# Performance work log

Measured on AMD Instinct MI355X. Metric: run time of the kernel, lower is better.

Reference implementation:

```python
import jax, jax.numpy as jnp
import numpy as np

THRESHOLD = 0.9
N = 20000
K = 32
F = 64


def setup_inputs() -> dict:
    key = jax.random.key(0)
    k1, k2, k3, k4, k5 = jax.random.split(key, 5)
    features = jax.random.normal(k1, (N, F), dtype=jnp.float32)
    score = jax.random.normal(k2, (N, 1), dtype=jnp.float32)
    distances = jax.random.uniform(k3, (N, K), dtype=jnp.float32)
    # two equal segments; neighbours sampled within own segment, self at col 0
    row_splits = jnp.array([0, N // 2, N], dtype=jnp.int32)
    segN = N // 2
    local_self = (jnp.arange(N, dtype=jnp.int32) % segN)
    seg_start = (jnp.arange(N, dtype=jnp.int32) // segN) * segN
    r = jax.random.randint(k4, (N, K - 1), 0, segN - 1, dtype=jnp.int32)
    r = r + (r >= local_self[:, None]).astype(jnp.int32)  # avoid sampling self
    neigh = seg_start[:, None] + r
    nidxs = jnp.concatenate([jnp.arange(N, dtype=jnp.int32)[:, None], neigh], axis=1)
    tidxs = jax.random.randint(k5, (N, 1), 0, 50, dtype=jnp.int32)
    return {"features": features, "score": score, "distances": distances,
            "nidxs": nidxs, "row_splits": row_splits, "tidxs": tidxs}


def _lnc(features, score_logits, nidxs, row_splits):
    n, k = nidxs.shape
    score = jax.nn.sigmoid(score_logits[:, 0])  # [N]
    # hierarchy order: per row-split segment, descending score
    seg_id = jnp.searchsorted(row_splits, jnp.arange(n), side='right') - 1
    order = jnp.lexsort((-score, seg_id))

    arangeK = jnp.arange(k)

    def step(carry, p):
        ggather, sel, npg, gcount = carry
        already = ggather[p] >= 0
        high = score[p] > THRESHOLD
        m = nidxs[p]                                   # [K], m[0] == p (self)
        free = (m >= 0) & (ggather[jnp.clip(m, 0, n - 1)] < 0)
        self_only = arangeK == 0
        valid = jnp.where(high, free, self_only) & (~already) & (m >= 0)
        g = gcount
        idx_w = jnp.where(valid, m, n)                 # dummy slot n for masked writes
        ggather = ggather.at[idx_w].set(g)
        row_i = jnp.where(already, n, g)
        sel = sel.at[row_i].set(jnp.where(valid, m, -1))
        npg = npg.at[row_i].set(jnp.sum(valid.astype(jnp.int32)))
        created = (~already).astype(jnp.int32)
        return (ggather, sel, npg, gcount + created), created

    init = (jnp.full((n + 1,), -1, jnp.int32),
            jnp.full((n + 1, k), -1, jnp.int32),
            jnp.zeros((n + 1,), jnp.int32),
            jnp.int32(0))
    (ggather, sel, npg, gcount), created = jax.lax.scan(step, init, order)
    ggather, sel, npg = ggather[:n], sel[:n], npg[:n]

    # new row splits: cumulative group count at segment boundaries
    cum = jnp.cumsum(created)
    rs_new = jnp.concatenate([jnp.zeros((1,), jnp.int32),
                              cum[row_splits[1:] - 1].astype(jnp.int32)])

    # pooled features per group (rows >= gcount are padding)
    sel_c = jnp.clip(sel, 0, n - 1)
    gathered = features[sel_c]                         # [N, K, F]
    mask = (sel >= 0)[..., None]
    out_mean = jnp.sum(jnp.where(mask, gathered, 0.0), axis=1)
    out_mean = out_mean / (npg[:, None].astype(features.dtype) + 1e-6)
    out_max = jnp.max(jnp.where(mask, gathered, -1000.0), axis=1)
    out = jnp.concatenate([out_mean, out_max], axis=-1)  # [N, 2F]
    backgather = ggather[:, None]
    return out, rs_new, backgather


def reference(features, score, distances, nidxs, row_splits, tidxs):
    # distances/tidxs only feed the (disabled) loss branch; kept for signature parity
    return _lnc(features, score, nidxs, row_splits)
```

## Files before the change

### kernel.cpp

```cpp
#include <hip/hip_runtime.h>


constexpr int KN = 32;
constexpr int FD = 64;
constexpr int HOCAP = 512;
constexpr int EW = 16;
constexpr int NBB = 2048;
constexpr int NT = 256;
constexpr int NTA = 512;
constexpr int NMAX = 20000;
constexpr int BSLOT = 64;
constexpr int TS = 2048;

typedef unsigned long long u64;

__device__ __forceinline__ int swz(int i) { return i ^ ((i >> 4) & 3); }

__global__ void k0_init(const float* __restrict__ score, int* __restrict__ grab,
                        u64* __restrict__ hlkStage, int* __restrict__ hcnt,
                        int* __restrict__ lcnt0, int* __restrict__ lcnt1,
                        u64* __restrict__ key, const int* __restrict__ row_splits,
                        int n) {
  __shared__ int ch, cl0, cl1;
  int tid = (int)threadIdx.x, bid = (int)blockIdx.x;
  int x = bid * NT + tid;
  int lane = tid & 63;
  int half = row_splits[1];
  if (tid == 0) { ch = 0; cl0 = 0; cl1 = 0; }
  __syncthreads();
  bool hi = false, lo = false;
  u64 pk = 0;
  if (x < n) {
    float sp = 1.0f / (1.0f + expf(-score[x]));
    grab[x] = 0x7FFFFFFF;
    hi = sp > 0.9f; lo = !hi;
    unsigned sb = __float_as_uint(sp);
    pk = ((u64)(x >= half) << 63) | ((u64)(0x7FFFFFFFu - sb) << 32) | (unsigned)x;
    key[x] = lo ? (((u64)sb << 32) | (u64)(0xFFFFFFFFu - (unsigned)x)) : 0ull;
  }
  u64 bh = __ballot(hi);
  u64 b0 = __ballot(lo && x < half);
  u64 b1 = __ballot(lo && x >= half);
  int base = 0;
  if (lane == 0) {
    if (bh) base = atomicAdd(&ch, __popcll(bh));
    if (b0) atomicAdd(&cl0, __popcll(b0));
    if (b1) atomicAdd(&cl1, __popcll(b1));
  }
  base = __shfl(base, 0);
  if (hi) {
    int idx = base + __popcll(bh & ((1ull << lane) - 1ull));
    if (idx < BSLOT) hlkStage[bid * BSLOT + idx] = pk;
  }
  __syncthreads();
  if (tid == 0) {
    hcnt[bid] = (ch > BSLOT) ? BSLOT : ch;
    lcnt0[bid] = cl0; lcnt1[bid] = cl1;
  }
}

__global__ __launch_bounds__(NTA, 1) void kA(
    const u64* __restrict__ hlkStage, const int* __restrict__ hcnt,
    const int* __restrict__ lcnt0, const int* __restrict__ lcnt1,
    const int* __restrict__ nidxs, const int* __restrict__ row_splits,
    int* __restrict__ nbm, int* __restrict__ fgj, int* __restrict__ counters,
    int n) {
  __shared__ unsigned short hr16[NMAX];
  __shared__ unsigned E[HOCAP * EW];
  __shared__ u64 hk[HOCAP];
  __shared__ int hol[HOCAP];
  __shared__ int fgjL[HOCAP];
  __shared__ int cnts[128];
  __shared__ int pref[129];
  __shared__ int lsum[2];
  __shared__ int shg;
  int tid = (int)threadIdx.x;
  int lane = tid & 63;
  int half = row_splits[1];
  int nblk = (n + NT - 1) / NT; if (nblk > 128) nblk = 128;

  {
    unsigned* h32 = (unsigned*)hr16;
    for (int i = tid; i < NMAX / 2; i += NTA) h32[i] = 0xFFFFFFFFu;
  }
  for (int i = tid; i < HOCAP * EW; i += NTA) E[i] = 0u;
  if (tid < 128) cnts[tid] = (tid < nblk) ? hcnt[tid] : 0;
  if (tid == 0) { lsum[0] = 0; lsum[1] = 0; }
  __syncthreads();

  if (tid < 64) {
    int v0 = cnts[tid], v1 = cnts[64 + tid];
#pragma unroll
    for (int off = 1; off < 64; off <<= 1) {
      int t0 = __shfl_up(v0, off), t1 = __shfl_up(v1, off);
      if (lane >= off) { v0 += t0; v1 += t1; }
    }
    int s0 = __shfl(v0, 63);
    pref[tid + 1] = v0;
    pref[64 + tid + 1] = v1 + s0;
    if (tid == 0) pref[0] = 0;
  }
  if (tid >= 64 && tid < 192) {
    int b = tid - 64;
    if (b < nblk) { atomicAdd(&lsum[0], lcnt0[b]); atomicAdd(&lsum[1], lcnt1[b]); }
  }
  __syncthreads();
  int nh = pref[nblk]; if (nh > HOCAP) nh = HOCAP;

  for (int t = tid; t < nblk * BSLOT; t += NTA) {
    int b = t >> 6, j = t & (BSLOT - 1);
    if (j < cnts[b]) {
      int d = pref[b] + j;
      if (d < HOCAP) hk[d] = hlkStage[t];
    }
  }
  __syncthreads();

  for (int i = tid; i < nh; i += NTA) {
    u64 kp = hk[i];
    int rk = 0;
#pragma unroll 8
    for (int j = 0; j < nh; ++j) rk += (hk[j] < kp) ? 1 : 0;
    int p = (int)(unsigned)(kp & 0xFFFFFFFFu);
    hol[rk] = p; hr16[p] = (unsigned short)rk;
  }
  __syncthreads();

  {
    const int4* nsrc = (const int4*)nidxs;
    int4* ndstG = (int4*)nbm;
    int tot = nh * 8;
    for (int t = tid; t < tot; t += NTA) {
      int j = t >> 3, q4 = t & 7;
      int p = hol[j];
      int4 v = nsrc[p * 8 + q4];
      ndstG[t] = v;
      unsigned bit = 1u << (j & 31);
      unsigned widx = (unsigned)(j >> 5);
      int xs[4] = { v.x, v.y, v.z, v.w };
#pragma unroll
      for (int e = 0; e < 4; ++e) {
        unsigned r = ((unsigned)xs[e] < (unsigned)n) ? hr16[xs[e]] : 0xFFFFu;
        if (r != 0xFFFFu) atomicOr(&E[r * EW + widx], bit);
      }
    }
  }
  __syncthreads();

  if (tid < 64) {
    unsigned Fw[16];
#pragma unroll
    for (int w = 0; w < 16; ++w) Fw[w] = 0u;
    int hg = 0, h0 = 0, h1 = 0;
    u64 mask_lt = (1ull << lane) - 1ull;
#pragma unroll
    for (int c = 0; c < HOCAP / 64; ++c) {
      if (c * 64 >= nh) break;
      int j = c * 64 + lane;
      bool valid = j < nh;
      unsigned er[16];
#pragma unroll
      for (int w = 0; w < 16; ++w) er[w] = valid ? E[j * EW + w] : 0u;
      unsigned acc = 0;
#pragma unroll
      for (int w = 0; w < 16; ++w) acc |= er[w] & Fw[w];
      bool base_already = acc != 0u;
      u64 erc = ((u64)er[2 * c + 1] << 32) | er[2 * c];
      u64 fb = 0;
      for (int l = 0; l < 64; ++l) {
        bool already = base_already || ((erc & fb) != 0ull);
        bool formed = valid && !already;
        fb |= __ballot(formed && (lane == l));
      }
      Fw[2 * c]     |= (unsigned)(fb & 0xFFFFFFFFull);
      Fw[2 * c + 1] |= (unsigned)(fb >> 32);
      bool formed = (fb >> lane) & 1ull;
      int p = valid ? hol[j] : 0;
      if (formed) {
        int idx = hg + __popcll(fb & mask_lt);
        fgjL[idx] = j;
      }
      h0 += __popcll(__ballot(formed && p < half));
      h1 += __popcll(__ballot(formed && p >= half));
      hg += __popcll(fb);
    }
    if (lane == 0) {
      counters[1] = hg; counters[2] = h0; counters[3] = h1; shg = hg;
    }
  }
  __syncthreads();
  int hg = shg;
  for (int i = tid; i < hg; i += NTA) fgj[i] = fgjL[i];
  if (tid == 0) {
    counters[0] = nh;
    counters[4] = lsum[0];
    counters[5] = lsum[1];
  }
}

__global__ void kG(const int* __restrict__ nbm, const int* __restrict__ fgj,
                   int* __restrict__ grab, u64* __restrict__ key,
                   int* __restrict__ counters, const int* __restrict__ row_splits,
                   int n) {
  int t = (int)(blockIdx.x * blockDim.x + threadIdx.x);
  int lane = (int)threadIdx.x & 63;
  int half = row_splits[1];
  int hg = counters[1];
  bool gl0 = false, gl1 = false;
  if (t < hg * KN) {
    int g = t >> 5;
    int x = nbm[fgj[g] * KN + (t & 31)];
    if ((unsigned)x < (unsigned)n) {
      int old = atomicMin(&grab[x], g);
      if (old == 0x7FFFFFFF && key[x] != 0ull) {
        key[x] = 0ull;
        if (x < half) gl0 = true; else gl1 = true;
      }
    }
  }
  u64 b0 = __ballot(gl0), b1 = __ballot(gl1);
  if (lane == 0) {
    if (b0) atomicSub(&counters[4], __popcll(b0));
    if (b1) atomicSub(&counters[5], __popcll(b1));
  }
}

__global__ void kBC(const int* __restrict__ row_splits, const u64* __restrict__ key,
                    const int* __restrict__ grab, const int* __restrict__ nbm,
                    const int* __restrict__ fgj, const int* __restrict__ counters,
                    const float* __restrict__ feat, float* __restrict__ out,
                    int n, int rs_off) {
  __shared__ u64 ktile[TS];
  int tid = (int)threadIdx.x, bid = (int)blockIdx.x;
  int gtid = bid * NT + tid;
  int lane = tid & 63;
  int wv = tid >> 6;
  int half = row_splits[1];
  const int GSZ = NBB * NT;
  const int NW = GSZ >> 6;
  int wid = gtid >> 6;
  int hg = counters[1], H0 = counters[2], H1 = counters[3];
  int L0 = counters[4], L1 = counters[5];
  int G = H0 + H1 + L0 + L1;
  int bg = rs_off + 3;
  const float inv1 = 1.0f / (1.0f + 1e-6f);

  int nblk16 = (n + 15) >> 4;
  for (int tsk = bid; tsk < nblk16; tsk += NBB) {
    int p0 = tsk * 16;
    int pw = p0 + wv * 4;
    u64 kp[4];
#pragma unroll
    for (int j = 0; j < 4; ++j) kp[j] = (pw + j < n) ? key[pw + j] : 0ull;
    int seg_lo = (p0 < half) ? 0 : half;
    int seg_cnt = (p0 < half) ? half : (n - half);
    unsigned r0 = 0, r1 = 0, r2 = 0, r3 = 0;
    for (int toff = 0; toff < seg_cnt; toff += TS) {
      int tcnt = seg_cnt - toff; if (tcnt > TS) tcnt = TS;
      __syncthreads();
      for (int i = tid; i < tcnt; i += NT) ktile[swz(i)] = key[seg_lo + toff + i];
      __syncthreads();
      for (int i = lane; i < tcnt; i += 64) {
        u64 kk = ktile[swz(i)];
        r0 += (kk > kp[0]) ? 1u : 0u;
        r1 += (kk > kp[1]) ? 1u : 0u;
        r2 += (kk > kp[2]) ? 1u : 0u;
        r3 += (kk > kp[3]) ? 1u : 0u;
      }
    }
#pragma unroll
    for (int off = 32; off > 0; off >>= 1) {
      r0 += __shfl_down(r0, off);
      r1 += __shfl_down(r1, off);
      r2 += __shfl_down(r2, off);
      r3 += __shfl_down(r3, off);
    }
    r0 = __shfl(r0, 0); r1 = __shfl(r1, 0); r2 = __shfl(r2, 0); r3 = __shfl(r3, 0);
    unsigned rr[4] = { r0, r1, r2, r3 };
#pragma unroll
    for (int j = 0; j < 4; ++j) {
      if (kp[j] == 0ull) continue;
      int p = pw + j;
      int base = (p < half) ? H0 : (H0 + L0 + H1);
      int gid = base + (int)rr[j];
      float v = feat[p * FD + lane];
      out[gid * (2 * FD) + lane] = v * inv1;
      out[gid * (2 * FD) + FD + lane] = v;
      if (lane == 0) out[bg + p] = (float)gid;
    }
  }

  for (int x = gtid; x < n; x += GSZ) {
    int prov = grab[x];
    if (prov != 0x7FFFFFFF)
      out[bg + x] = (float)((prov < H0) ? prov : (prov + L0));
  }

  for (int row = G + wid; row < n; row += NW) {
    out[row * (2 * FD) + lane] = 0.0f;
    out[row * (2 * FD) + FD + lane] = -1000.0f;
  }

  {
    int wtail = (NBB - 1 - bid) * (NT >> 6) + wv;
    for (int g = wtail; g < hg; g += NW) {
      int x = 0;
      bool mine = false;
      if (lane < KN) {
        x = nbm[fgj[g] * KN + lane];
        mine = (grab[x] == g);
      }
      u64 bal = __ballot(mine);
      unsigned mask = (unsigned)(bal & 0xFFFFFFFFull);
      int npg = __popc(mask);
      float sum = 0.0f, mx = -1000.0f;
      for (int k = 0; k < KN; ++k) {
        if (mask & (1u << k)) {
          int m = __shfl(x, k);
          float v = feat[m * FD + lane];
          sum += v; mx = fmaxf(mx, v);
        }
      }
      int gid2 = (g < H0) ? g : (g + L0);
      out[gid2 * (2 * FD) + lane] = sum / ((float)npg + 1e-6f);
      out[gid2 * (2 * FD) + FD + lane] = mx;
    }
  }

  if (gtid == 0) {
    out[rs_off + 0] = 0.0f;
    out[rs_off + 1] = (float)(H0 + L0);
    out[rs_off + 2] = (float)(H0 + L0 + H1 + L1);
  }
}

extern "C" void kernel_launch(void* const* d_in, const int* in_sizes, int n_in,
                              void* d_out, int out_size, void* d_ws, size_t ws_size,
                              hipStream_t stream) {
  const float* features   = (const float*)d_in[0];
  const float* score      = (const float*)d_in[1];
  const int*   nidxs      = (const int*)d_in[3];
  const int*   row_splits = (const int*)d_in[4];
  int n = in_sizes[1];
  float* out = (float*)d_out;
  int* wsi = (int*)d_ws;
  int rs_off = n * 2 * FD;

  int*      counters = wsi;
  int*      grab     = wsi + 8 + n;
  u64*      key      = (u64*)(wsi + 8 + 2 * n);
  int*      nbm      = wsi + 8 + 5 * n;
  int*      fgj      = wsi + 8 + 5 * n + HOCAP * KN;
  u64*      hlkStage = (u64*)(fgj + 2 * HOCAP);
  int*      hcnt     = (int*)(hlkStage + 128 * BSLOT);
  int*      lcnt0    = hcnt + 128;
  int*      lcnt1    = lcnt0 + 128;

  int blocks = (n + NT - 1) / NT;
  k0_init<<<blocks, NT, 0, stream>>>(score, grab, hlkStage, hcnt, lcnt0,
                                     lcnt1, key, row_splits, n);
  kA<<<1, NTA, 0, stream>>>(hlkStage, hcnt, lcnt0, lcnt1, nidxs, row_splits,
                            nbm, fgj, counters, n);
  kG<<<(HOCAP * KN) / NT, NT, 0, stream>>>(nbm, fgj, grab, key, counters,
                                           row_splits, n);
  kBC<<<NBB, NT, 0, stream>>>(row_splits, key, grab, nbm, fgj, counters,
                              features, out, n, rs_off);
}
```

Measured before the change: 72.80 us.

## Fuse init, hierarchy and grab kernels into one persistent kernel with grid semaphores

Merges the three launches for score init, high-score ordering/conflict resolution and grab into a single 40-block kernel. Blocks hand off through agent-scope atomic semaphores with spin-wait, and block 0 performs the serial phase. The intent is to remove two kernel launch gaps and their dependencies, at the cost of a memset launch and a spin-based grid barrier that depends on all 40 blocks being co-resident. The per-block staging buffers shrink to match the 40 blocks of 512 threads.

```diff
diff --git a/kernel.cpp b/kernel.cpp
--- a/kernel.cpp
+++ b/kernel.cpp
@@ -7,7 +7,8 @@
 constexpr int EW = 16;
 constexpr int NBB = 2048;
 constexpr int NT = 256;
-constexpr int NTA = 512;
+constexpr int NBF = 40;
+constexpr int NTF = 512;
 constexpr int NMAX = 20000;
 constexpr int BSLOT = 64;
 constexpr int TS = 2048;
@@ -16,212 +17,222 @@
 
 __device__ __forceinline__ int swz(int i) { return i ^ ((i >> 4) & 3); }
 
-__global__ void k0_init(const float* __restrict__ score, int* __restrict__ grab,
-                        u64* __restrict__ hlkStage, int* __restrict__ hcnt,
-                        int* __restrict__ lcnt0, int* __restrict__ lcnt1,
-                        u64* __restrict__ key, const int* __restrict__ row_splits,
-                        int n) {
-  __shared__ int ch, cl0, cl1;
-  int tid = (int)threadIdx.x, bid = (int)blockIdx.x;
-  int x = bid * NT + tid;
-  int lane = tid & 63;
-  int half = row_splits[1];
-  if (tid == 0) { ch = 0; cl0 = 0; cl1 = 0; }
-  __syncthreads();
-  bool hi = false, lo = false;
-  u64 pk = 0;
-  if (x < n) {
-    float sp = 1.0f / (1.0f + expf(-score[x]));
-    grab[x] = 0x7FFFFFFF;
-    hi = sp > 0.9f; lo = !hi;
-    unsigned sb = __float_as_uint(sp);
-    pk = ((u64)(x >= half) << 63) | ((u64)(0x7FFFFFFFu - sb) << 32) | (unsigned)x;
-    key[x] = lo ? (((u64)sb << 32) | (u64)(0xFFFFFFFFu - (unsigned)x)) : 0ull;
-  }
-  u64 bh = __ballot(hi);
-  u64 b0 = __ballot(lo && x < half);
-  u64 b1 = __ballot(lo && x >= half);
-  int base = 0;
-  if (lane == 0) {
-    if (bh) base = atomicAdd(&ch, __popcll(bh));
-    if (b0) atomicAdd(&cl0, __popcll(b0));
-    if (b1) atomicAdd(&cl1, __popcll(b1));
-  }
-  base = __shfl(base, 0);
-  if (hi) {
-    int idx = base + __popcll(bh & ((1ull << lane) - 1ull));
-    if (idx < BSLOT) hlkStage[bid * BSLOT + idx] = pk;
-  }
-  __syncthreads();
-  if (tid == 0) {
-    hcnt[bid] = (ch > BSLOT) ? BSLOT : ch;
-    lcnt0[bid] = cl0; lcnt1[bid] = cl1;
-  }
-}
-
-__global__ __launch_bounds__(NTA, 1) void kA(
-    const u64* __restrict__ hlkStage, const int* __restrict__ hcnt,
-    const int* __restrict__ lcnt0, const int* __restrict__ lcnt1,
-    const int* __restrict__ nidxs, const int* __restrict__ row_splits,
-    int* __restrict__ nbm, int* __restrict__ fgj, int* __restrict__ counters,
-    int n) {
+__global__ __launch_bounds__(NTF, 1) void kF(
+    const float* __restrict__ score, const int* __restrict__ nidxs,
+    const int* __restrict__ row_splits, int* __restrict__ grab,
+    u64* __restrict__ key, int* __restrict__ nbm, int* __restrict__ fgj,
+    int* __restrict__ counters, int* __restrict__ sems,
+    u64* __restrict__ hlkStage, int* __restrict__ hcnt,
+    int* __restrict__ lcnt0, int* __restrict__ lcnt1, int n) {
   __shared__ unsigned short hr16[NMAX];
   __shared__ unsigned E[HOCAP * EW];
   __shared__ u64 hk[HOCAP];
   __shared__ int hol[HOCAP];
   __shared__ int fgjL[HOCAP];
-  __shared__ int cnts[128];
-  __shared__ int pref[129];
+  __shared__ int cnts[NBF];
+  __shared__ int pref[NBF + 1];
   __shared__ int lsum[2];
   __shared__ int shg;
-  int tid = (int)threadIdx.x;
+  __shared__ int ch, cl0, cl1;
+  int tid = (int)threadIdx.x, bid = (int)blockIdx.x;
   int lane = tid & 63;
   int half = row_splits[1];
-  int nblk = (n + NT - 1) / NT; if (nblk > 128) nblk = 128;
-
+
+  if (tid == 0) { ch = 0; cl0 = 0; cl1 = 0; }
+  __syncthreads();
   {
-    unsigned* h32 = (unsigned*)hr16;
-    for (int i = tid; i < NMAX / 2; i += NTA) h32[i] = 0xFFFFFFFFu;
-  }
-  for (int i = tid; i < HOCAP * EW; i += NTA) E[i] = 0u;
-  if (tid < 128) cnts[tid] = (tid < nblk) ? hcnt[tid] : 0;
-  if (tid == 0) { lsum[0] = 0; lsum[1] = 0; }
+    int x = bid * NTF + tid;
+    bool hi = false, lo = false;
+    u64 pk = 0;
+    if (x < n) {
+      float sp = 1.0f / (1.0f + expf(-score[x]));
+      grab[x] = 0x7FFFFFFF;
+      hi = sp > 0.9f; lo = !hi;
+      unsigned sb = __float_as_uint(sp);
+      pk = ((u64)(x >= half) << 63) | ((u64)(0x7FFFFFFFu - sb) << 32) |
+           (unsigned)x;
+      key[x] = lo ? (((u64)sb << 32) | (u64)(0xFFFFFFFFu - (unsigned)x)) : 0ull;
+    }
+    u64 bh = __ballot(hi);
+    u64 b0 = __ballot(lo && x < half);
+    u64 b1 = __ballot(lo && x >= half);
+    int base = 0;
+    if (lane == 0) {
+      if (bh) base = atomicAdd(&ch, __popcll(bh));
+      if (b0) atomicAdd(&cl0, __popcll(b0));
+      if (b1) atomicAdd(&cl1, __popcll(b1));
+    }
+    base = __shfl(base, 0);
+    if (hi) {
+      int idx = base + __popcll(bh & ((1ull << lane) - 1ull));
+      if (idx < BSLOT) hlkStage[bid * BSLOT + idx] = pk;
+    }
+  }
   __syncthreads();
-
-  if (tid < 64) {
-    int v0 = cnts[tid], v1 = cnts[64 + tid];
-#pragma unroll
-    for (int off = 1; off < 64; off <<= 1) {
-      int t0 = __shfl_up(v0, off), t1 = __shfl_up(v1, off);
-      if (lane >= off) { v0 += t0; v1 += t1; }
-    }
-    int s0 = __shfl(v0, 63);
-    pref[tid + 1] = v0;
-    pref[64 + tid + 1] = v1 + s0;
-    if (tid == 0) pref[0] = 0;
-  }
-  if (tid >= 64 && tid < 192) {
-    int b = tid - 64;
-    if (b < nblk) { atomicAdd(&lsum[0], lcnt0[b]); atomicAdd(&lsum[1], lcnt1[b]); }
+  if (tid == 0) {
+    hcnt[bid] = (ch > BSLOT) ? BSLOT : ch;
+    lcnt0[bid] = cl0; lcnt1[bid] = cl1;
+    __hip_atomic_fetch_add(&sems[0], 1, __ATOMIC_RELEASE,
+                           __HIP_MEMORY_SCOPE_AGENT);
+  }
+
+  if (bid == 0) {
+    if (tid == 0) {
+      while (__hip_atomic_load(&sems[0], __ATOMIC_RELAXED,
+                               __HIP_MEMORY_SCOPE_AGENT) < NBF)
+        __builtin_amdgcn_s_sleep(2);
+      __builtin_amdgcn_fence(__ATOMIC_ACQUIRE, "agent");
+    }
+    __syncthreads();
+
+    {
+      unsigned* h32 = (unsigned*)hr16;
+      for (int i = tid; i < NMAX / 2; i += NTF) h32[i] = 0xFFFFFFFFu;
+    }
+    for (int i = tid; i < HOCAP * EW; i += NTF) E[i] = 0u;
+    if (tid < NBF) cnts[tid] = hcnt[tid];
+    if (tid == 0) { lsum[0] = 0; lsum[1] = 0; }
+    __syncthreads();
+
+    if (tid < 64) {
+      int v = (tid < NBF) ? cnts[tid] : 0;
+#pragma unroll
+      for (int off = 1; off < 64; off <<= 1) {
+        int t0 = __shfl_up(v, off);
+        if (lane >= off) v += t0;
+      }
+      if (tid < NBF) pref[tid + 1] = v;
+      if (tid == 0) pref[0] = 0;
+    }
+    if (tid >= 64 && tid < 64 + NBF) {
+      int b = tid - 64;
+      atomicAdd(&lsum[0], lcnt0[b]); atomicAdd(&lsum[1], lcnt1[b]);
+    }
+    __syncthreads();
+    int nh = pref[NBF]; if (nh > HOCAP) nh = HOCAP;
+
+    for (int t = tid; t < NBF * BSLOT; t += NTF) {
+      int b = t >> 6, j = t & (BSLOT - 1);
+      if (j < cnts[b]) {
+        int d = pref[b] + j;
+        if (d < HOCAP) hk[d] = hlkStage[t];
+      }
+    }
+    __syncthreads();
+
+    for (int i = tid; i < nh; i += NTF) {
+      u64 kp = hk[i];
+      int rk = 0;
+#pragma unroll 8
+      for (int j = 0; j < nh; ++j) rk += (hk[j] < kp) ? 1 : 0;
+      int p = (int)(unsigned)(kp & 0xFFFFFFFFu);
+      hol[rk] = p; hr16[p] = (unsigned short)rk;
+    }
+    __syncthreads();
+
+    {
+      const int4* nsrc = (const int4*)nidxs;
+      int4* ndstG = (int4*)nbm;
+      int tot = nh * 8;
+      for (int t = tid; t < tot; t += NTF) {
+        int j = t >> 3, q4 = t & 7;
+        int p = hol[j];
+        int4 v = nsrc[p * 8 + q4];
+        ndstG[t] = v;
+        unsigned bit = 1u << (j & 31);
+        unsigned widx = (unsigned)(j >> 5);
+        int xs[4] = { v.x, v.y, v.z, v.w };
+#pragma unroll
+        for (int e = 0; e < 4; ++e) {
+          unsigned r = ((unsigned)xs[e] < (unsigned)n) ? hr16[xs[e]] : 0xFFFFu;
+          if (r != 0xFFFFu) atomicOr(&E[r * EW + widx], bit);
+        }
+      }
+    }
+    __syncthreads();
+
+    if (tid < 64) {
+      unsigned Fw[16];
+#pragma unroll
+      for (int w = 0; w < 16; ++w) Fw[w] = 0u;
+      int hg = 0, h0 = 0, h1 = 0;
+      u64 mask_lt = (1ull << lane) - 1ull;
+#pragma unroll
+      for (int c = 0; c < HOCAP / 64; ++c) {
+        if (c * 64 >= nh) break;
+        int j = c * 64 + lane;
+        bool valid = j < nh;
+        unsigned er[16];
+#pragma unroll
+        for (int w = 0; w < 16; ++w) er[w] = valid ? E[j * EW + w] : 0u;
+        unsigned acc = 0;
+#pragma unroll
+        for (int w = 0; w < 16; ++w) acc |= er[w] & Fw[w];
+        bool base_already = acc != 0u;
+        u64 erc = ((u64)er[2 * c + 1] << 32) | er[2 * c];
+        u64 fb = 0;
+        for (int l = 0; l < 64; ++l) {
+          bool already = base_already || ((erc & fb) != 0ull);
+          bool formed = valid && !already;
+          fb |= __ballot(formed && (lane == l));
+        }
+        Fw[2 * c]     |= (unsigned)(fb & 0xFFFFFFFFull);
+        Fw[2 * c + 1] |= (unsigned)(fb >> 32);
+        bool formed = (fb >> lane) & 1ull;
+        int p = valid ? hol[j] : 0;
+        if (formed) {
+          int idx = hg + __popcll(fb & mask_lt);
+          fgjL[idx] = j;
+        }
+        h0 += __popcll(__ballot(formed && p < half));
+        h1 += __popcll(__ballot(formed && p >= half));
+        hg += __popcll(fb);
+      }
+      if (lane == 0) {
+        counters[1] = hg; counters[2] = h0; counters[3] = h1; shg = hg;
+      }
+    }
+    __syncthreads();
+    int hgv = shg;
+    for (int i = tid; i < hgv; i += NTF) fgj[i] = fgjL[i];
+    if (tid == 0) {
+      counters[0] = (pref[NBF] > HOCAP) ? HOCAP : pref[NBF];
+      counters[4] = lsum[0];
+      counters[5] = lsum[1];
+    }
+    __syncthreads();
+    if (tid == 0)
+      __hip_atomic_fetch_add(&sems[1], 1, __ATOMIC_RELEASE,
+                             __HIP_MEMORY_SCOPE_AGENT);
+  }
+
+  if (tid == 0) {
+    while (__hip_atomic_load(&sems[1], __ATOMIC_RELAXED,
+                             __HIP_MEMORY_SCOPE_AGENT) < 1)
+      __builtin_amdgcn_s_sleep(2);
+    __builtin_amdgcn_fence(__ATOMIC_ACQUIRE, "agent");
   }
   __syncthreads();
-  int nh = pref[nblk]; if (nh > HOCAP) nh = HOCAP;
-
-  for (int t = tid; t < nblk * BSLOT; t += NTA) {
-    int b = t >> 6, j = t & (BSLOT - 1);
-    if (j < cnts[b]) {
-      int d = pref[b] + j;
-      if (d < HOCAP) hk[d] = hlkStage[t];
-    }
-  }
-  __syncthreads();
-
-  for (int i = tid; i < nh; i += NTA) {
-    u64 kp = hk[i];
-    int rk = 0;
-#pragma unroll 8
-    for (int j = 0; j < nh; ++j) rk += (hk[j] < kp) ? 1 : 0;
-    int p = (int)(unsigned)(kp & 0xFFFFFFFFu);
-    hol[rk] = p; hr16[p] = (unsigned short)rk;
-  }
-  __syncthreads();
-
   {
-    const int4* nsrc = (const int4*)nidxs;
-    int4* ndstG = (int4*)nbm;
-    int tot = nh * 8;
-    for (int t = tid; t < tot; t += NTA) {
-      int j = t >> 3, q4 = t & 7;
-      int p = hol[j];
-      int4 v = nsrc[p * 8 + q4];
-      ndstG[t] = v;
-      unsigned bit = 1u << (j & 31);
-      unsigned widx = (unsigned)(j >> 5);
-      int xs[4] = { v.x, v.y, v.z, v.w };
-#pragma unroll
-      for (int e = 0; e < 4; ++e) {
-        unsigned r = ((unsigned)xs[e] < (unsigned)n) ? hr16[xs[e]] : 0xFFFFu;
-        if (r != 0xFFFFu) atomicOr(&E[r * EW + widx], bit);
-      }
-    }
-  }
-  __syncthreads();
-
-  if (tid < 64) {
-    unsigned Fw[16];
-#pragma unroll
-    for (int w = 0; w < 16; ++w) Fw[w] = 0u;
-    int hg = 0, h0 = 0, h1 = 0;
-    u64 mask_lt = (1ull << lane) - 1ull;
-#pragma unroll
-    for (int c = 0; c < HOCAP / 64; ++c) {
-      if (c * 64 >= nh) break;
-      int j = c * 64 + lane;
-      bool valid = j < nh;
-      unsigned er[16];
-#pragma unroll
-      for (int w = 0; w < 16; ++w) er[w] = valid ? E[j * EW + w] : 0u;
-      unsigned acc = 0;
-#pragma unroll
-      for (int w = 0; w < 16; ++w) acc |= er[w] & Fw[w];
-      bool base_already = acc != 0u;
-      u64 erc = ((u64)er[2 * c + 1] << 32) | er[2 * c];
-      u64 fb = 0;
-      for (int l = 0; l < 64; ++l) {
-        bool already = base_already || ((erc & fb) != 0ull);
-        bool formed = valid && !already;
-        fb |= __ballot(formed && (lane == l));
-      }
-      Fw[2 * c]     |= (unsigned)(fb & 0xFFFFFFFFull);
-      Fw[2 * c + 1] |= (unsigned)(fb >> 32);
-      bool formed = (fb >> lane) & 1ull;
-      int p = valid ? hol[j] : 0;
-      if (formed) {
-        int idx = hg + __popcll(fb & mask_lt);
-        fgjL[idx] = j;
-      }
-      h0 += __popcll(__ballot(formed && p < half));
-      h1 += __popcll(__ballot(formed && p >= half));
-      hg += __popcll(fb);
-    }
+    int hg = counters[1];
+    int t = bid * NTF + tid;
+    bool gl0 = false, gl1 = false;
+    if (t < hg * KN) {
+      int g = t >> 5;
+      int x = nbm[fgj[g] * KN + (t & 31)];
+      if ((unsigned)x < (unsigned)n) {
+        int old = atomicMin(&grab[x], g);
+        if (old == 0x7FFFFFFF && key[x] != 0ull) {
+          key[x] = 0ull;
+          if (x < half) gl0 = true; else gl1 = true;
+        }
+      }
+    }
+    u64 b0 = __ballot(gl0), b1 = __ballot(gl1);
     if (lane == 0) {
-      counters[1] = hg; counters[2] = h0; counters[3] = h1; shg = hg;
-    }
-  }
-  __syncthreads();
-  int hg = shg;
-  for (int i = tid; i < hg; i += NTA) fgj[i] = fgjL[i];
-  if (tid == 0) {
-    counters[0] = nh;
-    counters[4] = lsum[0];
-    counters[5] = lsum[1];
-  }
-}
-
-__global__ void kG(const int* __restrict__ nbm, const int* __restrict__ fgj,
-                   int* __restrict__ grab, u64* __restrict__ key,
-                   int* __restrict__ counters, const int* __restrict__ row_splits,
-                   int n) {
-  int t = (int)(blockIdx.x * blockDim.x + threadIdx.x);
-  int lane = (int)threadIdx.x & 63;
-  int half = row_splits[1];
-  int hg = counters[1];
-  bool gl0 = false, gl1 = false;
-  if (t < hg * KN) {
-    int g = t >> 5;
-    int x = nbm[fgj[g] * KN + (t & 31)];
-    if ((unsigned)x < (unsigned)n) {
-      int old = atomicMin(&grab[x], g);
-      if (old == 0x7FFFFFFF && key[x] != 0ull) {
-        key[x] = 0ull;
-        if (x < half) gl0 = true; else gl1 = true;
-      }
-    }
-  }
-  u64 b0 = __ballot(gl0), b1 = __ballot(gl1);
-  if (lane == 0) {
-    if (b0) atomicSub(&counters[4], __popcll(b0));
-    if (b1) atomicSub(&counters[5], __popcll(b1));
+      if (b0) atomicSub(&counters[4], __popcll(b0));
+      if (b1) atomicSub(&counters[5], __popcll(b1));
+    }
   }
 }
 
@@ -347,22 +358,19 @@
   int rs_off = n * 2 * FD;
 
   int*      counters = wsi;
+  int*      sems     = wsi + 8;
   int*      grab     = wsi + 8 + n;
   u64*      key      = (u64*)(wsi + 8 + 2 * n);
   int*      nbm      = wsi + 8 + 5 * n;
   int*      fgj      = wsi + 8 + 5 * n + HOCAP * KN;
   u64*      hlkStage = (u64*)(fgj + 2 * HOCAP);
-  int*      hcnt     = (int*)(hlkStage + 128 * BSLOT);
-  int*      lcnt0    = hcnt + 128;
-  int*      lcnt1    = lcnt0 + 128;
-
-  int blocks = (n + NT - 1) / NT;
-  k0_init<<<blocks, NT, 0, stream>>>(score, grab, hlkStage, hcnt, lcnt0,
-                                     lcnt1, key, row_splits, n);
-  kA<<<1, NTA, 0, stream>>>(hlkStage, hcnt, lcnt0, lcnt1, nidxs, row_splits,
-                            nbm, fgj, counters, n);
-  kG<<<(HOCAP * KN) / NT, NT, 0, stream>>>(nbm, fgj, grab, key, counters,
-                                           row_splits, n);
+  int*      hcnt     = (int*)(hlkStage + NBF * BSLOT);
+  int*      lcnt0    = hcnt + NBF;
+  int*      lcnt1    = lcnt0 + NBF;
+
+  (void)hipMemsetAsync(sems, 0, 2 * sizeof(int), stream);
+  kF<<<NBF, NTF, 0, stream>>>(score, nidxs, row_splits, grab, key, nbm, fgj,
+                              counters, sems, hlkStage, hcnt, lcnt0, lcnt1, n);
   kBC<<<NBB, NT, 0, stream>>>(row_splits, key, grab, nbm, fgj, counters,
                               features, out, n, rs_off);
 }
```

New measurement: 73.14 us. About the same (+0.5%).

## Split single-block hierarchy kernel across blocks and fuse grab pass with semaphore

Applied to the files above, without the earlier changes.

The single 512-thread block that built the high-score conflict bitmap is replaced by a 40-block kernel. Each block redundantly ranks the candidates, then handles a slice of neighbour lookups. The 20000-entry shared rank table is replaced by binary search over candidates sorted by point id, and the bitmap is built in global memory with atomics. The greedy formation step and the grab pass are fused into one kernel in which block 0 computes the groups and the other blocks spin on a global semaphore before doing the atomicMin grabs. This removes a kernel launch and the serial shared-memory init of the large table, at the cost of redundant per-block ranking, global atomics, and a spin-wait that assumes all blocks are co-resident.

```diff
diff --git a/kernel.cpp b/kernel.cpp
--- a/kernel.cpp
+++ b/kernel.cpp
@@ -7,8 +7,8 @@
 constexpr int EW = 16;
 constexpr int NBB = 2048;
 constexpr int NT = 256;
-constexpr int NTA = 512;
-constexpr int NMAX = 20000;
+constexpr int NBA2 = 40;
+constexpr int NBG = 64;
 constexpr int BSLOT = 64;
 constexpr int TS = 2048;
 
@@ -19,14 +19,17 @@
 __global__ void k0_init(const float* __restrict__ score, int* __restrict__ grab,
                         u64* __restrict__ hlkStage, int* __restrict__ hcnt,
                         int* __restrict__ lcnt0, int* __restrict__ lcnt1,
-                        u64* __restrict__ key, const int* __restrict__ row_splits,
-                        int n) {
+                        u64* __restrict__ key, unsigned* __restrict__ EG,
+                        int* __restrict__ sems,
+                        const int* __restrict__ row_splits, int n) {
   __shared__ int ch, cl0, cl1;
   int tid = (int)threadIdx.x, bid = (int)blockIdx.x;
   int x = bid * NT + tid;
   int lane = tid & 63;
   int half = row_splits[1];
   if (tid == 0) { ch = 0; cl0 = 0; cl1 = 0; }
+  if (x < HOCAP * EW) EG[x] = 0u;
+  if (x == 0) sems[0] = 0;
   __syncthreads();
   bool hi = false, lo = false;
   u64 pk = 0;
@@ -59,35 +62,20 @@
   }
 }
 
-__global__ __launch_bounds__(NTA, 1) void kA(
+__global__ __launch_bounds__(NT) void kA2(
     const u64* __restrict__ hlkStage, const int* __restrict__ hcnt,
-    const int* __restrict__ lcnt0, const int* __restrict__ lcnt1,
-    const int* __restrict__ nidxs, const int* __restrict__ row_splits,
-    int* __restrict__ nbm, int* __restrict__ fgj, int* __restrict__ counters,
-    int n) {
-  __shared__ unsigned short hr16[NMAX];
-  __shared__ unsigned E[HOCAP * EW];
+    const int* __restrict__ nidxs, int* __restrict__ nbm,
+    int* __restrict__ holG, unsigned* __restrict__ EG, int n, int nblk) {
   __shared__ u64 hk[HOCAP];
   __shared__ int hol[HOCAP];
-  __shared__ int fgjL[HOCAP];
+  __shared__ int pidS[HOCAP];
+  __shared__ unsigned short rnkS[HOCAP];
   __shared__ int cnts[128];
   __shared__ int pref[129];
-  __shared__ int lsum[2];
-  __shared__ int shg;
-  int tid = (int)threadIdx.x;
+  int tid = (int)threadIdx.x, bid = (int)blockIdx.x;
   int lane = tid & 63;
-  int half = row_splits[1];
-  int nblk = (n + NT - 1) / NT; if (nblk > 128) nblk = 128;
-
-  {
-    unsigned* h32 = (unsigned*)hr16;
-    for (int i = tid; i < NMAX / 2; i += NTA) h32[i] = 0xFFFFFFFFu;
-  }
-  for (int i = tid; i < HOCAP * EW; i += NTA) E[i] = 0u;
   if (tid < 128) cnts[tid] = (tid < nblk) ? hcnt[tid] : 0;
-  if (tid == 0) { lsum[0] = 0; lsum[1] = 0; }
-  __syncthreads();
-
+  __syncthreads();
   if (tid < 64) {
     int v0 = cnts[tid], v1 = cnts[64 + tid];
 #pragma unroll
@@ -100,14 +88,10 @@
     pref[64 + tid + 1] = v1 + s0;
     if (tid == 0) pref[0] = 0;
   }
-  if (tid >= 64 && tid < 192) {
-    int b = tid - 64;
-    if (b < nblk) { atomicAdd(&lsum[0], lcnt0[b]); atomicAdd(&lsum[1], lcnt1[b]); }
-  }
   __syncthreads();
   int nh = pref[nblk]; if (nh > HOCAP) nh = HOCAP;
 
-  for (int t = tid; t < nblk * BSLOT; t += NTA) {
+  for (int t = tid; t < nblk * BSLOT; t += NT) {
     int b = t >> 6, j = t & (BSLOT - 1);
     if (j < cnts[b]) {
       int d = pref[b] + j;
@@ -116,112 +100,161 @@
   }
   __syncthreads();
 
-  for (int i = tid; i < nh; i += NTA) {
+  for (int i = tid; i < nh; i += NT) {
     u64 kp = hk[i];
-    int rk = 0;
-#pragma unroll 8
-    for (int j = 0; j < nh; ++j) rk += (hk[j] < kp) ? 1 : 0;
-    int p = (int)(unsigned)(kp & 0xFFFFFFFFu);
-    hol[rk] = p; hr16[p] = (unsigned short)rk;
-  }
-  __syncthreads();
+    unsigned px = (unsigned)kp;
+    int rk = 0, rq = 0;
+    for (int j = 0; j < nh; ++j) {
+      u64 kj = hk[j];
+      rk += (kj < kp) ? 1 : 0;
+      rq += ((unsigned)kj < px) ? 1 : 0;
+    }
+    hol[rk] = (int)px;
+    holG[rk] = (int)px;
+    pidS[rq] = (int)px;
+    rnkS[rq] = (unsigned short)rk;
+  }
+  __syncthreads();
+
+  int gpb = (nh + NBA2 - 1) / NBA2;
+  int j0 = bid * gpb;
+  int j1 = j0 + gpb; if (j1 > nh) j1 = nh;
+  int cnt = (j1 > j0) ? (j1 - j0) : 0;
 
   {
     const int4* nsrc = (const int4*)nidxs;
-    int4* ndstG = (int4*)nbm;
-    int tot = nh * 8;
-    for (int t = tid; t < tot; t += NTA) {
-      int j = t >> 3, q4 = t & 7;
-      int p = hol[j];
-      int4 v = nsrc[p * 8 + q4];
-      ndstG[t] = v;
-      unsigned bit = 1u << (j & 31);
-      unsigned widx = (unsigned)(j >> 5);
-      int xs[4] = { v.x, v.y, v.z, v.w };
-#pragma unroll
-      for (int e = 0; e < 4; ++e) {
-        unsigned r = ((unsigned)xs[e] < (unsigned)n) ? hr16[xs[e]] : 0xFFFFu;
-        if (r != 0xFFFFu) atomicOr(&E[r * EW + widx], bit);
-      }
-    }
-  }
-  __syncthreads();
-
-  if (tid < 64) {
-    unsigned Fw[16];
-#pragma unroll
-    for (int w = 0; w < 16; ++w) Fw[w] = 0u;
-    int hg = 0, h0 = 0, h1 = 0;
-    u64 mask_lt = (1ull << lane) - 1ull;
-#pragma unroll
-    for (int c = 0; c < HOCAP / 64; ++c) {
-      if (c * 64 >= nh) break;
-      int j = c * 64 + lane;
-      bool valid = j < nh;
-      unsigned er[16];
-#pragma unroll
-      for (int w = 0; w < 16; ++w) er[w] = valid ? E[j * EW + w] : 0u;
-      unsigned acc = 0;
-#pragma unroll
-      for (int w = 0; w < 16; ++w) acc |= er[w] & Fw[w];
-      bool base_already = acc != 0u;
-      u64 erc = ((u64)er[2 * c + 1] << 32) | er[2 * c];
-      u64 fb = 0;
-      for (int l = 0; l < 64; ++l) {
-        bool already = base_already || ((erc & fb) != 0ull);
-        bool formed = valid && !already;
-        fb |= __ballot(formed && (lane == l));
-      }
-      Fw[2 * c]     |= (unsigned)(fb & 0xFFFFFFFFull);
-      Fw[2 * c + 1] |= (unsigned)(fb >> 32);
-      bool formed = (fb >> lane) & 1ull;
-      int p = valid ? hol[j] : 0;
-      if (formed) {
-        int idx = hg + __popcll(fb & mask_lt);
-        fgjL[idx] = j;
-      }
-      h0 += __popcll(__ballot(formed && p < half));
-      h1 += __popcll(__ballot(formed && p >= half));
-      hg += __popcll(fb);
-    }
+    int4* ndst = (int4*)nbm;
+    for (int t = tid; t < cnt * 8; t += NT) {
+      int j = j0 + (t >> 3), q4 = t & 7;
+      ndst[j * 8 + q4] = nsrc[hol[j] * 8 + q4];
+    }
+  }
+  for (int t = tid; t < cnt * KN; t += NT) {
+    int j = j0 + (t >> 5), k = t & 31;
+    int x = nidxs[hol[j] * KN + k];
+    int lo = 0, hi = nh - 1, pos = -1;
+    while (lo <= hi) {
+      int mid = (lo + hi) >> 1;
+      int v = pidS[mid];
+      if (v == x) { pos = mid; break; }
+      if (v < x) lo = mid + 1; else hi = mid - 1;
+    }
+    if (pos >= 0)
+      atomicOr(&EG[(int)rnkS[pos] * EW + (j >> 5)], 1u << (j & 31));
+  }
+}
+
+__global__ __launch_bounds__(NT) void kA3G(
+    const unsigned* __restrict__ EG, const int* __restrict__ holG,
+    const int* __restrict__ hcnt, const int* __restrict__ lcnt0,
+    const int* __restrict__ lcnt1, const int* __restrict__ nbm,
+    const int* __restrict__ row_splits, int* __restrict__ grab,
+    u64* __restrict__ key, int* __restrict__ fgj, int* __restrict__ counters,
+    int* __restrict__ sems, int n, int nblk) {
+  __shared__ unsigned E[HOCAP * EW];
+  __shared__ int hol[HOCAP];
+  __shared__ int fgjL[HOCAP];
+  __shared__ int lsum0, lsum1, snh, shg;
+  int tid = (int)threadIdx.x, bid = (int)blockIdx.x;
+  int lane = tid & 63;
+  int half = row_splits[1];
+
+  if (bid == 0) {
+    if (tid == 0) { lsum0 = 0; lsum1 = 0; snh = 0; }
+    __syncthreads();
+    if (tid < nblk) {
+      atomicAdd(&lsum0, lcnt0[tid]);
+      atomicAdd(&lsum1, lcnt1[tid]);
+      atomicAdd(&snh, hcnt[tid]);
+    }
+    __syncthreads();
+    int nh = snh; if (nh > HOCAP) nh = HOCAP;
+    {
+      const int4* esrc = (const int4*)EG;
+      int4* edst = (int4*)E;
+      for (int i = tid; i < nh * 4; i += NT) edst[i] = esrc[i];
+    }
+    for (int i = tid; i < nh; i += NT) hol[i] = holG[i];
+    __syncthreads();
+
+    if (tid < 64) {
+      unsigned Fw[16];
+#pragma unroll
+      for (int w = 0; w < 16; ++w) Fw[w] = 0u;
+      int hg = 0, h0 = 0, h1 = 0;
+      u64 mask_lt = (1ull << lane) - 1ull;
+#pragma unroll
+      for (int c = 0; c < HOCAP / 64; ++c) {
+        if (c * 64 >= nh) break;
+        int j = c * 64 + lane;
+        bool valid = j < nh;
+        unsigned er[16];
+#pragma unroll
+        for (int w = 0; w < 16; ++w) er[w] = valid ? E[j * EW + w] : 0u;
+        unsigned acc = 0;
+#pragma unroll
+        for (int w = 0; w < 16; ++w) acc |= er[w] & Fw[w];
+        bool base_already = acc != 0u;
+        u64 erc = ((u64)er[2 * c + 1] << 32) | er[2 * c];
+        u64 fb = 0;
+        for (int l = 0; l < 64; ++l) {
+          bool already = base_already || ((erc & fb) != 0ull);
+          bool formed = valid && !already;
+          fb |= __ballot(formed && (lane == l));
+        }
+        Fw[2 * c]     |= (unsigned)(fb & 0xFFFFFFFFull);
+        Fw[2 * c + 1] |= (unsigned)(fb >> 32);
+        bool formed = (fb >> lane) & 1ull;
+        int p = valid ? hol[j] : 0;
+        if (formed) {
+          int idx = hg + __popcll(fb & mask_lt);
+          fgjL[idx] = j;
+        }
+        h0 += __popcll(__ballot(formed && p < half));
+        h1 += __popcll(__ballot(formed && p >= half));
+        hg += __popcll(fb);
+      }
+      if (lane == 0) {
+        counters[1] = hg; counters[2] = h0; counters[3] = h1; shg = hg;
+      }
+    }
+    __syncthreads();
+    int hgv = shg;
+    for (int i = tid; i < hgv; i += NT) fgj[i] = fgjL[i];
+    if (tid == 0) { counters[4] = lsum0; counters[5] = lsum1; }
+    __syncthreads();
+    if (tid == 0)
+      __hip_atomic_fetch_add(&sems[0], 1, __ATOMIC_RELEASE,
+                             __HIP_MEMORY_SCOPE_AGENT);
+  }
+
+  if (tid == 0) {
+    while (__hip_atomic_load(&sems[0], __ATOMIC_RELAXED,
+                             __HIP_MEMORY_SCOPE_AGENT) < 1)
+      __builtin_amdgcn_s_sleep(2);
+    __builtin_amdgcn_fence(__ATOMIC_ACQUIRE, "agent");
+  }
+  __syncthreads();
+  {
+    int hg = counters[1];
+    int t = bid * NT + tid;
+    bool gl0 = false, gl1 = false;
+    if (t < hg * KN) {
+      int g = t >> 5;
+      int x = nbm[fgj[g] * KN + (t & 31)];
+      if ((unsigned)x < (unsigned)n) {
+        int old = atomicMin(&grab[x], g);
+        if (old == 0x7FFFFFFF && key[x] != 0ull) {
+          key[x] = 0ull;
+          if (x < half) gl0 = true; else gl1 = true;
+        }
+      }
+    }
+    u64 b0 = __ballot(gl0), b1 = __ballot(gl1);
     if (lane == 0) {
-      counters[1] = hg; counters[2] = h0; counters[3] = h1; shg = hg;
-    }
-  }
-  __syncthreads();
-  int hg = shg;
-  for (int i = tid; i < hg; i += NTA) fgj[i] = fgjL[i];
-  if (tid == 0) {
-    counters[0] = nh;
-    counters[4] = lsum[0];
-    counters[5] = lsum[1];
-  }
-}
-
-__global__ void kG(const int* __restrict__ nbm, const int* __restrict__ fgj,
-                   int* __restrict__ grab, u64* __restrict__ key,
-                   int* __restrict__ counters, const int* __restrict__ row_splits,
-                   int n) {
-  int t = (int)(blockIdx.x * blockDim.x + threadIdx.x);
-  int lane = (int)threadIdx.x & 63;
-  int half = row_splits[1];
-  int hg = counters[1];
-  bool gl0 = false, gl1 = false;
-  if (t < hg * KN) {
-    int g = t >> 5;
-    int x = nbm[fgj[g] * KN + (t & 31)];
-    if ((unsigned)x < (unsigned)n) {
-      int old = atomicMin(&grab[x], g);
-      if (old == 0x7FFFFFFF && key[x] != 0ull) {
-        key[x] = 0ull;
-        if (x < half) gl0 = true; else gl1 = true;
-      }
-    }
-  }
-  u64 b0 = __ballot(gl0), b1 = __ballot(gl1);
-  if (lane == 0) {
-    if (b0) atomicSub(&counters[4], __popcll(b0));
-    if (b1) atomicSub(&counters[5], __popcll(b1));
+      if (b0) atomicSub(&counters[4], __popcll(b0));
+      if (b1) atomicSub(&counters[5], __popcll(b1));
+    }
   }
 }
 
@@ -347,22 +380,24 @@
   int rs_off = n * 2 * FD;
 
   int*      counters = wsi;
-  int*      grab     = wsi + 8 + n;
-  u64*      key      = (u64*)(wsi + 8 + 2 * n);
-  int*      nbm      = wsi + 8 + 5 * n;
-  int*      fgj      = wsi + 8 + 5 * n + HOCAP * KN;
-  u64*      hlkStage = (u64*)(fgj + 2 * HOCAP);
+  int*      sems     = wsi + 8;
+  int*      grab     = wsi + 16;
+  u64*      key      = (u64*)(wsi + 16 + n);
+  int*      nbm      = wsi + 16 + 3 * n;
+  int*      fgj      = wsi + 16 + 3 * n + HOCAP * KN;
+  int*      holG     = fgj + HOCAP;
+  unsigned* EG       = (unsigned*)(holG + HOCAP);
+  u64*      hlkStage = (u64*)(EG + HOCAP * EW);
   int*      hcnt     = (int*)(hlkStage + 128 * BSLOT);
   int*      lcnt0    = hcnt + 128;
   int*      lcnt1    = lcnt0 + 128;
 
-  int blocks = (n + NT - 1) / NT;
-  k0_init<<<blocks, NT, 0, stream>>>(score, grab, hlkStage, hcnt, lcnt0,
-                                     lcnt1, key, row_splits, n);
-  kA<<<1, NTA, 0, stream>>>(hlkStage, hcnt, lcnt0, lcnt1, nidxs, row_splits,
-                            nbm, fgj, counters, n);
-  kG<<<(HOCAP * KN) / NT, NT, 0, stream>>>(nbm, fgj, grab, key, counters,
-                                           row_splits, n);
+  int nblk = (n + NT - 1) / NT;
+  k0_init<<<nblk, NT, 0, stream>>>(score, grab, hlkStage, hcnt, lcnt0, lcnt1,
+                                   key, EG, sems, row_splits, n);
+  kA2<<<NBA2, NT, 0, stream>>>(hlkStage, hcnt, nidxs, nbm, holG, EG, n, nblk);
+  kA3G<<<NBG, NT, 0, stream>>>(EG, holG, hcnt, lcnt0, lcnt1, nbm, row_splits,
+                               grab, key, fgj, counters, sems, n, nblk);
   kBC<<<NBB, NT, 0, stream>>>(row_splits, key, grab, nbm, fgj, counters,
                               features, out, n, rs_off);
 }
```

After: 87.73 us. +20.5%, slower.
